# Optimization experiments

Hardware: AMD Instinct MI355X
Metric: run time of the kernel (lower is better)

The kernel has to match this reference:

```python
import jax, jax.numpy as jnp
import numpy as np

# hyperparameters from init_kwargs
TEMP = 0.05
MOMENTUM = 0.2
ALPHA = 0.9
TEMP_DIST = 0.6
LAMBDA1 = 1.0
LAMBDA2 = 1.0
EPS_CONS = 2.0
NUM_SAMPLES = 8192
NUM_FEATURES = 2048
B = 256
K = 20
EPS = 1e-12


def setup_inputs() -> dict:
    key = jax.random.key(0)
    ks = jax.random.split(key, 8)
    inputs0 = jax.random.normal(ks[0], (B, NUM_FEATURES), dtype=jnp.float32)
    logits0 = jax.random.normal(ks[1], (B, NUM_SAMPLES), dtype=jnp.float32)
    logits1 = jax.random.normal(ks[2], (B, NUM_SAMPLES), dtype=jnp.float32)
    targets = jax.random.randint(ks[3], (B,), 0, NUM_SAMPLES, dtype=jnp.int32)
    indexes = jnp.arange(B, dtype=jnp.int32)  # global idx == batch idx (identity idx2bidx)
    neighbors = jax.random.randint(ks[4], (B, K), 0, B, dtype=jnp.int32)
    neighbor_dists = jax.random.uniform(ks[5], (B, K), dtype=jnp.float32)
    rampup = jnp.ones((), dtype=jnp.float32)
    features = jax.random.normal(ks[6], (NUM_SAMPLES, NUM_FEATURES), dtype=jnp.float32)
    features = features / jnp.linalg.norm(features, axis=1, keepdims=True)
    return {
        'inputs0': inputs0, 'logits0': logits0, 'logits1': logits1,
        'targets': targets, 'indexes': indexes, 'neighbors': neighbors,
        'neighbor_dists': neighbor_dists, 'rampup': rampup, 'features': features,
    }


def reference(inputs0, logits0, logits1, targets, indexes, neighbors,
              neighbor_dists, rampup, features):
    # F.normalize(inputs[0], dim=1)
    x = inputs0 / jnp.maximum(jnp.linalg.norm(inputs0, axis=1, keepdims=True), EPS)

    # CM forward: scores against memory bank, scaled by temperature
    outputs = (x @ features.T) / TEMP                      # [B, S]
    logp = jax.nn.log_softmax(outputs, axis=-1)
    loss_nce = -jnp.mean(jnp.take_along_axis(logp, targets[:, None], axis=1))

    targets_onehot = jax.nn.one_hot(targets, NUM_SAMPLES, dtype=logits0.dtype)

    # neighbor gathering: indexes = arange(B) so idx2bidx is identity; every
    # neighbor in [0,B) passes the `nb in indexes` filter.
    p0 = jax.nn.softmax(logits0, axis=-1)[neighbors]       # [B, K, S]
    p1 = jax.nn.softmax(logits1, axis=-1)[neighbors]       # [B, K, S]
    # loop appends logits0-row then logits1-row per neighbor -> interleave
    p = jnp.stack([p0, p1], axis=2).reshape(B, 2 * K, NUM_SAMPLES)
    d2 = jnp.repeat(neighbor_dists, 2, axis=1)             # [B, 2K] (d,d pairs)
    w = jax.nn.softmax(d2 / TEMP_DIST, axis=1)             # [B, 2K]
    logits_neighbors1 = jnp.einsum('bk,bks->bs', w, p)     # [B, S]

    # KL branch: neighbors with dist <= eps_consistency (all, since eps=2.0)
    mask = (neighbor_dists <= EPS_CONS).astype(p0.dtype)   # [B, K]
    cnt = jnp.maximum(mask.sum(axis=1, keepdims=True), 1.0)
    logits_neighbors1_KL = jnp.einsum('bk,bks->bs', mask, p0) / cnt  # [B, S]

    refined = ALPHA * targets_onehot + (1.0 - ALPHA) * jax.lax.stop_gradient(logits_neighbors1)
    loss_ce = jnp.mean(jnp.sum(-refined * jax.nn.log_softmax(logits0, axis=-1), axis=1))

    # KLDivLoss(logsoftmax(logits1).detach(), target) with batchmean reduction
    lp1 = jax.lax.stop_gradient(jax.nn.log_softmax(logits1, axis=-1))
    t = logits_neighbors1_KL
    kl = jnp.sum(jnp.where(t > 0, t * (jnp.log(jnp.maximum(t, EPS)) - lp1), 0.0)) / B

    # CM momentum memory-bank scatter update (backward side-effect in torch);
    # equivalent to the sequential loop when targets are unique in the batch.
    upd = MOMENTUM * features[targets] + (1.0 - MOMENTUM) * x
    upd = upd / jnp.maximum(jnp.linalg.norm(upd, axis=1, keepdims=True), EPS)
    new_features = features.at[targets].set(upd)

    return (loss_nce, LAMBDA1 * loss_ce, LAMBDA2 * rampup * kl, new_features)
```

## Files before the change

### kernel.cpp

```cpp
#include <hip/hip_runtime.h>
#include <cmath>

#define NB 256
#define NS 8192
#define NF 2048
#define NK 20

typedef _Float16 half8 __attribute__((ext_vector_type(8)));
typedef _Float16 half4 __attribute__((ext_vector_type(4)));
typedef float f32x4 __attribute__((ext_vector_type(4)));

__device__ __forceinline__ void async16(const void* g, void* l) {
  __builtin_amdgcn_global_load_lds(
      (const __attribute__((address_space(1))) unsigned int*)g,
      (__attribute__((address_space(3))) unsigned int*)l, 16, 0, 0);
}

__device__ __forceinline__ float waveSum(float v) {
#pragma unroll
  for (int off = 32; off > 0; off >>= 1) v += __shfl_xor(v, off, 64);
  return v;
}
__device__ __forceinline__ float waveMax(float v) {
#pragma unroll
  for (int off = 32; off > 0; off >>= 1) v = fmaxf(v, __shfl_xor(v, off, 64));
  return v;
}

__global__ __launch_bounds__(256, 1) void prep(
    const float4* __restrict__ f4, const float* __restrict__ in0,
    const float* __restrict__ logits0, const float* __restrict__ logits1,
    const int* __restrict__ targets, const int* __restrict__ neighbors,
    const float* __restrict__ ndist,
    float* __restrict__ outF, _Float16* __restrict__ fh,
    _Float16* __restrict__ Pt, _Float16* __restrict__ xh,
    _Float16* __restrict__ alpha_h, float* __restrict__ mll,
    _Float16* __restrict__ Wp) {
  __shared__ alignas(16) union {
    struct {
      float redA[4];
      float redB[4];
      unsigned long long wmask[4];
    } s;
    _Float16 Lt[32 * 520];
  } sm;
  int tid = threadIdx.x, blk = blockIdx.x;
  int wave = tid >> 6, lane = tid & 63;

  if (blk < NS) {
    int row = blk;
    const float4* fr = f4 + (size_t)row * (NF / 4);
    float4 v0 = fr[tid], v1 = fr[tid + 256];
    half4 h0, h1;
    h0[0] = (_Float16)v0.x; h0[1] = (_Float16)v0.y; h0[2] = (_Float16)v0.z; h0[3] = (_Float16)v0.w;
    h1[0] = (_Float16)v1.x; h1[1] = (_Float16)v1.y; h1[2] = (_Float16)v1.z; h1[3] = (_Float16)v1.w;
    ((half4*)(fh + (size_t)row * NF))[tid] = h0;
    ((half4*)(fh + (size_t)row * NF))[tid + 256] = h1;
    unsigned long long mk = __ballot(targets[tid] == row);
    if (lane == 0) sm.s.wmask[wave] = mk;
    __syncthreads();
    int u = -1;
#pragma unroll
    for (int w = 3; w >= 0; --w)
      if (u < 0 && sm.s.wmask[w])
        u = w * 64 + 63 - (int)__clzll(sm.s.wmask[w]);
    if (u >= 0) {
      const float4* xr = (const float4*)(in0 + (size_t)u * NF);
      float4 a0 = xr[tid], a1 = xr[tid + 256];
      float ssx = a0.x * a0.x + a0.y * a0.y + a0.z * a0.z + a0.w * a0.w +
                  a1.x * a1.x + a1.y * a1.y + a1.z * a1.z + a1.w * a1.w;
      float w1 = waveSum(ssx);
      if (lane == 0) sm.s.redA[wave] = w1;
      __syncthreads();
      float totx = (sm.s.redA[0] + sm.s.redA[1]) + (sm.s.redA[2] + sm.s.redA[3]);
      float ix = 0.8f / fmaxf(sqrtf(totx), 1e-12f);
      v0 = make_float4(0.2f * v0.x + ix * a0.x, 0.2f * v0.y + ix * a0.y,
                       0.2f * v0.z + ix * a0.z, 0.2f * v0.w + ix * a0.w);
      v1 = make_float4(0.2f * v1.x + ix * a1.x, 0.2f * v1.y + ix * a1.y,
                       0.2f * v1.z + ix * a1.z, 0.2f * v1.w + ix * a1.w);
      float ss = v0.x * v0.x + v0.y * v0.y + v0.z * v0.z + v0.w * v0.w +
                 v1.x * v1.x + v1.y * v1.y + v1.z * v1.z + v1.w * v1.w;
      float w2 = waveSum(ss);
      if (lane == 0) sm.s.redB[wave] = w2;
      __syncthreads();
      float tot = (sm.s.redB[0] + sm.s.redB[1]) + (sm.s.redB[2] + sm.s.redB[3]);
      float inv = 1.0f / fmaxf(sqrtf(tot), 1e-12f);
      v0.x *= inv; v0.y *= inv; v0.z *= inv; v0.w *= inv;
      v1.x *= inv; v1.y *= inv; v1.z *= inv; v1.w *= inv;
    }
    float* o = outF + (size_t)row * NF;
    int e0 = tid * 4, e1 = 1024 + tid * 4;
    o[e0 + 0] = v0.x; o[e0 + 1] = v0.y; o[e0 + 2] = v0.z; o[e0 + 3] = v0.w;
    o[e1 + 0] = v1.x; o[e1 + 1] = v1.y; o[e1 + 2] = v1.z; o[e1 + 3] = v1.w;
  } else if (blk < NS + 512) {
    int r = blk - NS;
    const float* src = (r < NB) ? logits0 : logits1;
    const float4* row = (const float4*)(src + (size_t)(r & (NB - 1)) * NS);
    float4 v[8];
    float mx = -1e30f;
#pragma unroll
    for (int i = 0; i < 8; ++i) {
      v[i] = row[tid + i * 256];
      mx = fmaxf(mx, fmaxf(fmaxf(v[i].x, v[i].y), fmaxf(v[i].z, v[i].w)));
    }
    float wv = waveMax(mx);
    if (lane == 0) sm.s.redA[wave] = wv;
    __syncthreads();
    float m = fmaxf(fmaxf(sm.s.redA[0], sm.s.redA[1]), fmaxf(sm.s.redA[2], sm.s.redA[3]));
    float se = 0.0f;
#pragma unroll
    for (int i = 0; i < 8; ++i)
      se += expf(v[i].x - m) + expf(v[i].y - m) + expf(v[i].z - m) + expf(v[i].w - m);
    float sw = waveSum(se);
    if (lane == 0) sm.s.redB[wave] = sw;
    __syncthreads();
    float l = (sm.s.redB[0] + sm.s.redB[1]) + (sm.s.redB[2] + sm.s.redB[3]);
    if (tid == 0) {
      mll[r] = m + logf(l);
      alpha_h[r] = (_Float16)(256.0f * expf(-m) / l);
    }
  } else if (blk < NS + 768) {
    int s0 = (blk - (NS + 512)) * 32;
#pragma unroll
    for (int g = 0; g < 16; ++g) {
      int pos = g * 256 + tid;
      int row = pos >> 3, c4 = pos & 7;
      const float* src = ((row < NB) ? logits0 + (size_t)row * NS
                                     : logits1 + (size_t)(row - NB) * NS) + s0 + c4 * 4;
      float4 v = *(const float4*)src;
      sm.Lt[(c4 * 4 + 0) * 520 + row] = (_Float16)expf(v.x);
      sm.Lt[(c4 * 4 + 1) * 520 + row] = (_Float16)expf(v.y);
      sm.Lt[(c4 * 4 + 2) * 520 + row] = (_Float16)expf(v.z);
      sm.Lt[(c4 * 4 + 3) * 520 + row] = (_Float16)expf(v.w);
    }
    __syncthreads();
    int srow = tid >> 3, seg = tid & 7;
    _Float16* dst = Pt + (size_t)(s0 + srow) * 512 + seg * 64;
    const _Float16* lsrc = &sm.Lt[srow * 520 + seg * 64];
#pragma unroll
    for (int q = 0; q < 8; ++q)
      *(half8*)(dst + q * 8) = *(const half8*)(lsrc + q * 8);
  } else if (blk < NS + 1024) {
    int b = blk - (NS + 768);
    const float4* row = (const float4*)(in0 + (size_t)b * NF);
    float4 v0 = row[tid], v1 = row[tid + 256];
    float ss = v0.x * v0.x + v0.y * v0.y + v0.z * v0.z + v0.w * v0.w +
               v1.x * v1.x + v1.y * v1.y + v1.z * v1.z + v1.w * v1.w;
    float w = waveSum(ss);
    if (lane == 0) sm.s.redA[wave] = w;
    __syncthreads();
    float tot = (sm.s.redA[0] + sm.s.redA[1]) + (sm.s.redA[2] + sm.s.redA[3]);
    float inv = 1.0f / fmaxf(sqrtf(tot), 1e-12f);
    half4 h0, h1;
    h0[0] = (_Float16)(v0.x * inv); h0[1] = (_Float16)(v0.y * inv);
    h0[2] = (_Float16)(v0.z * inv); h0[3] = (_Float16)(v0.w * inv);
    h1[0] = (_Float16)(v1.x * inv); h1[1] = (_Float16)(v1.y * inv);
    h1[2] = (_Float16)(v1.z * inv); h1[3] = (_Float16)(v1.w * inv);
    ((half4*)(xh + (size_t)b * NF))[tid] = h0;
    ((half4*)(xh + (size_t)b * NF))[tid + 256] = h1;
  } else {
    float4* W4 = (float4*)Wp;
    for (int i = tid; i < 512 * 512 * 2 / 16; i += 256) W4[i] = make_float4(0, 0, 0, 0);
    __syncthreads();
    int b = tid;
    float d[NK], e[NK];
    int n[NK];
    float s = 0.0f;
    int cnt = 0;
#pragma unroll
    for (int k = 0; k < NK; ++k) {
      d[k] = ndist[b * NK + k];
      n[k] = neighbors[b * NK + k];
      e[k] = expf(d[k] * (1.0f / 0.6f));
      s += e[k];
      cnt += (d[k] <= 2.0f) ? 1 : 0;
    }
    float invs = 1.0f / (2.0f * s);
    float invc = 1.0f / fmaxf((float)cnt, 1.0f);
    _Float16* rkl = Wp + (size_t)b * 512;
    _Float16* rce = Wp + (size_t)(256 + b) * 512;
#pragma unroll
    for (int k = 0; k < NK; ++k) {
      bool first = true;
#pragma unroll
      for (int k2 = 0; k2 < NK; ++k2)
        if (k2 < k && n[k2] == n[k]) first = false;
      if (first) {
        float wsum = 0.0f, ksum = 0.0f;
#pragma unroll
        for (int k2 = 0; k2 < NK; ++k2)
          if (k2 >= k && n[k2] == n[k]) {
            wsum += e[k2] * invs;
            ksum += (d[k2] <= 2.0f) ? invc : 0.0f;
          }
        rkl[n[k]] = (_Float16)ksum;
        rce[n[k]] = (_Float16)wsum;
        rce[256 + n[k]] = (_Float16)wsum;
      }
    }
  }
}

__global__ __launch_bounds__(256) void gemms(
    const _Float16* __restrict__ xh, const _Float16* __restrict__ fh,
    const _Float16* __restrict__ Wp, const _Float16* __restrict__ Pt,
    const _Float16* __restrict__ alpha_h,
    const float* __restrict__ logits0, const float* __restrict__ logits1,
    const float* __restrict__ mll, const int* __restrict__ targets,
    float* __restrict__ pm, float* __restrict__ pl, float* __restrict__ tgt,
    float* __restrict__ part) {
  __shared__ alignas(16) _Float16 As[128 * 64];
  __shared__ alignas(16) _Float16 Bs[128 * 64];
  __shared__ alignas(16) _Float16 Al[512];
  __shared__ float red[4];
  int tid = threadIdx.x, wave = tid >> 6, lane = tid & 63;
  int quad = lane >> 4, r16 = lane & 15, lrow = lane >> 3, lch = lane & 7;
  int blk = blockIdx.x;
  if (blk < 256) {
    int bx = blk & 127, by = blk >> 7;
    int n0 = bx * 64, m0 = by * 128;
    f32x4 acc[2][4] = {};
    for (int k0 = 0; k0 < NF; k0 += 64) {
      __syncthreads();
#pragma unroll
      for (int ss = 0; ss < 4; ++ss) {
        int rl = ss * 32 + wave * 8 + lrow;
        int sc = lch ^ (rl & 7);
        async16(xh + (size_t)(m0 + rl) * NF + k0 + sc * 8, &As[rl * 64 + lch * 8]);
      }
#pragma unroll
      for (int ss = 0; ss < 2; ++ss) {
        int rl = ss * 32 + wave * 8 + lrow;
        int sc = lch ^ (rl & 7);
        async16(fh + (size_t)(n0 + rl) * NF + k0 + sc * 8, &Bs[rl * 64 + lch * 8]);
      }
      __syncthreads();
#pragma unroll
      for (int sub = 0; sub < 2; ++sub) {
        int slot = ((sub * 4 + quad) ^ (r16 & 7)) * 8;
        half8 af[2], bf[4];
#pragma unroll
        for (int i = 0; i < 2; ++i)
          af[i] = *(const half8*)&As[(wave * 32 + i * 16 + r16) * 64 + slot];
#pragma unroll
        for (int j = 0; j < 4; ++j)
          bf[j] = *(const half8*)&Bs[(j * 16 + r16) * 64 + slot];
#pragma unroll
        for (int i = 0; i < 2; ++i)
#pragma unroll
          for (int j = 0; j < 4; ++j)
            acc[i][j] = __builtin_amdgcn_mfma_f32_16x16x32_f16(af[i], bf[j], acc[i][j], 0, 0, 0);
      }
    }
#pragma unroll
    for (int i = 0; i < 2; ++i)
#pragma unroll
      for (int r = 0; r < 4; ++r) {
        int R = m0 + wave * 32 + i * 16 + quad * 4 + r;
        float sv[4];
#pragma unroll
        for (int j = 0; j < 4; ++j) sv[j] = acc[i][j][r] * 20.0f;
        float mx = fmaxf(fmaxf(sv[0], sv[1]), fmaxf(sv[2], sv[3]));
#pragma unroll
        for (int m2 = 1; m2 < 16; m2 <<= 1) mx = fmaxf(mx, __shfl_xor(mx, m2, 64));
        float e = expf(sv[0] - mx) + expf(sv[1] - mx) + expf(sv[2] - mx) + expf(sv[3] - mx);
#pragma unroll
        for (int m2 = 1; m2 < 16; m2 <<= 1) e += __shfl_xor(e, m2, 64);
        int tg = targets[R];
#pragma unroll
        for (int j = 0; j < 4; ++j)
          if (n0 + j * 16 + r16 == tg) tgt[R] = sv[j];
        if (r16 == 0) { pm[R * 128 + bx] = mx; pl[R * 128 + bx] = e; }
      }
  } else {
    int nb = blk - 256;
    int bx = nb & 63, by = nb >> 6;
    int n0 = bx * 128, m0 = by * 128;
    int wm = (wave >> 1) * 64, wn = (wave & 1) * 64;
    if (tid < 64) ((half8*)Al)[tid] = ((const half8*)alpha_h)[tid];
    f32x4 acc[4][4] = {};
    for (int k0 = 0; k0 < 512; k0 += 64) {
      __syncthreads();
#pragma unroll
      for (int ss = 0; ss < 4; ++ss) {
        int rl = ss * 32 + wave * 8 + lrow;
        int sc = lch ^ (rl & 7);
        async16(Wp + (size_t)(m0 + rl) * 512 + k0 + sc * 8, &As[rl * 64 + lch * 8]);
        async16(Pt + (size_t)(n0 + rl) * 512 + k0 + sc * 8, &Bs[rl * 64 + lch * 8]);
      }
      __syncthreads();
#pragma unroll
      for (int sub = 0; sub < 2; ++sub) {
        int slot = ((sub * 4 + quad) ^ (r16 & 7)) * 8;
        half8 alv = *(const half8*)&Al[k0 + slot];
        half8 af[4], bf[4];
#pragma unroll
        for (int i = 0; i < 4; ++i)
          af[i] = *(const half8*)&As[(wm + i * 16 + r16) * 64 + slot];
#pragma unroll
        for (int j = 0; j < 4; ++j)
          bf[j] = *(const half8*)&Bs[(wn + j * 16 + r16) * 64 + slot] * alv;
#pragma unroll
        for (int i = 0; i < 4; ++i)
#pragma unroll
          for (int j = 0; j < 4; ++j)
            acc[i][j] = __builtin_amdgcn_mfma_f32_16x16x32_f16(af[i], bf[j], acc[i][j], 0, 0, 0);
      }
    }
    bool iskl = (by < 2);
    const float* lgbase = iskl ? logits1 : logits0;
    float local = 0.0f;
#pragma unroll
    for (int i = 0; i < 4; ++i)
#pragma unroll
      for (int r = 0; r < 4; ++r) {
        int Mg = m0 + wm + i * 16 + quad * 4 + r;
        int b = iskl ? Mg : (Mg - 256);
        float mv = mll[iskl ? 256 + b : b];
        const float* lgrow = lgbase + (size_t)b * NS + n0 + wn;
#pragma unroll
        for (int j = 0; j < 4; ++j) {
          float lg = lgrow[j * 16 + r16];
          float t = acc[i][j][r] * (1.0f / 256.0f);
          if (iskl)
            local += (t > 0.0f) ? t * (logf(fmaxf(t, 1e-12f)) - (lg - mv)) : 0.0f;
          else
            local += -0.1f * t * (lg - mv);
        }
      }
    float wsv = waveSum(local);
    if (lane == 0) red[wave] = wsv;
    __syncthreads();
    if (tid == 0) part[nb] = (red[0] + red[1]) + (red[2] + red[3]);
  }
}

__global__ __launch_bounds__(256) void final_reduce(
    const float* __restrict__ pm, const float* __restrict__ pl,
    const float* __restrict__ tgt, const float* __restrict__ part,
    const float* __restrict__ logits0, const float* __restrict__ mll,
    const int* __restrict__ targets, const float* __restrict__ rampup,
    float* __restrict__ out) {
  __shared__ float rA[4], rB[4], rC[4], rD[4];
  int tid = threadIdx.x, wave = tid >> 6, lane = tid & 63;
  int b = tid;
  const float* pmb = pm + b * 128;
  const float* plb = pl + b * 128;
  float mx = -1e30f;
  for (int s = 0; s < 128; ++s) mx = fmaxf(mx, pmb[s]);
  float S = 0.0f;
  for (int s = 0; s < 128; ++s) S += plb[s] * expf(pmb[s] - mx);
  float nce = -(tgt[b] - mx - logf(S));
  int tg = targets[b];
  float oh = -0.9f * (logits0[(size_t)b * NS + tg] - mll[b]);
  float c = part[tid];
  float klc = (tid < 128) ? c : 0.0f;
  float cec = (tid < 128) ? 0.0f : c;
  float wn_ = waveSum(nce), wo = waveSum(oh), wk = waveSum(klc), wc = waveSum(cec);
  if (lane == 0) { rA[wave] = wn_; rB[wave] = wo; rC[wave] = wk; rD[wave] = wc; }
  __syncthreads();
  if (tid == 0) {
    float sn = rA[0] + rA[1] + rA[2] + rA[3];
    float so = rB[0] + rB[1] + rB[2] + rB[3];
    float sk = rC[0] + rC[1] + rC[2] + rC[3];
    float sc2 = rD[0] + rD[1] + rD[2] + rD[3];
    out[0] = sn * (1.0f / 256.0f);
    out[1] = (so + sc2) * (1.0f / 256.0f);
    out[2] = rampup[0] * sk * (1.0f / 256.0f);
  }
}

extern "C" void kernel_launch(void* const* d_in, const int* in_sizes, int n_in,
                              void* d_out, int out_size, void* d_ws, size_t ws_size,
                              hipStream_t stream) {
  const float* inputs0 = (const float*)d_in[0];
  const float* logits0 = (const float*)d_in[1];
  const float* logits1 = (const float*)d_in[2];
  const int* targets = (const int*)d_in[3];
  const int* neighbors = (const int*)d_in[5];
  const float* ndist = (const float*)d_in[6];
  const float* rampup = (const float*)d_in[7];
  const float* features = (const float*)d_in[8];
  float* out = (float*)d_out;

  char* ws = (char*)d_ws;
  float* mll = (float*)(ws + 4096);
  _Float16* alpha_h = (_Float16*)(ws + 8192);
  float* part = (float*)(ws + 12288);
  float* tgt = (float*)(ws + 16384);
  float* pm = (float*)(ws + 65536);
  float* pl = (float*)(ws + 196608);
  _Float16* Wp = (_Float16*)(ws + 524288);
  _Float16* xh = (_Float16*)(ws + (3 << 20));
  _Float16* Pt = (_Float16*)(ws + (4 << 20));
  _Float16* fh = (_Float16*)(ws + (12 << 20));

  prep<<<NS + 1025, 256, 0, stream>>>((const float4*)features, inputs0, logits0,
                                      logits1, targets, neighbors, ndist,
                                      out + 3, fh, Pt, xh, alpha_h, mll, Wp);
  gemms<<<512, 256, 0, stream>>>(xh, fh, Wp, Pt, alpha_h, logits0, logits1, mll,
                                 targets, pm, pl, tgt, part);
  final_reduce<<<1, 256, 0, stream>>>(pm, pl, tgt, part, logits0, mll, targets,
                                      rampup, out);
}
```

Before: 220.3 us.

## Parallelize final reduction across blocks with atomics and split transpose blocks finer

The final loss reduction moves from a single 256-thread block, where each thread serially looped over 128 partials, to 256 blocks of 128 threads. Each block reduces one batch row with wave shuffles and accumulates into the outputs with atomicAdd; the outputs are zeroed inside prep. The logits exp/transpose stage now uses 512 blocks of 16 columns instead of 256 blocks of 32, which halves the shared tile and gives more parallel blocks. The memory-bank writeback is vectorized to float4 stores. Atomics make the summation order nondeterministic.

```diff
diff --git a/kernel.cpp b/kernel.cpp
--- a/kernel.cpp
+++ b/kernel.cpp
@@ -35,14 +35,14 @@
     float* __restrict__ outF, _Float16* __restrict__ fh,
     _Float16* __restrict__ Pt, _Float16* __restrict__ xh,
     _Float16* __restrict__ alpha_h, float* __restrict__ mll,
-    _Float16* __restrict__ Wp) {
+    _Float16* __restrict__ Wp, float* __restrict__ loss) {
   __shared__ alignas(16) union {
     struct {
       float redA[4];
       float redB[4];
       unsigned long long wmask[4];
     } s;
-    _Float16 Lt[32 * 520];
+    _Float16 Lt[16 * 520];
   } sm;
   int tid = threadIdx.x, blk = blockIdx.x;
   int wave = tid >> 6, lane = tid & 63;
@@ -88,10 +88,9 @@
       v0.x *= inv; v0.y *= inv; v0.z *= inv; v0.w *= inv;
       v1.x *= inv; v1.y *= inv; v1.z *= inv; v1.w *= inv;
     }
-    float* o = outF + (size_t)row * NF;
-    int e0 = tid * 4, e1 = 1024 + tid * 4;
-    o[e0 + 0] = v0.x; o[e0 + 1] = v0.y; o[e0 + 2] = v0.z; o[e0 + 3] = v0.w;
-    o[e1 + 0] = v1.x; o[e1 + 1] = v1.y; o[e1 + 2] = v1.z; o[e1 + 3] = v1.w;
+    float4* o4 = (float4*)(outF + (size_t)row * NF);
+    o4[tid] = v0;
+    o4[tid + 256] = v1;
   } else if (blk < NS + 512) {
     int r = blk - NS;
     const float* src = (r < NB) ? logits0 : logits1;
@@ -119,12 +118,12 @@
       mll[r] = m + logf(l);
       alpha_h[r] = (_Float16)(256.0f * expf(-m) / l);
     }
-  } else if (blk < NS + 768) {
-    int s0 = (blk - (NS + 512)) * 32;
-#pragma unroll
-    for (int g = 0; g < 16; ++g) {
+  } else if (blk < NS + 1024) {
+    int s0 = (blk - (NS + 512)) * 16;
+#pragma unroll
+    for (int g = 0; g < 8; ++g) {
       int pos = g * 256 + tid;
-      int row = pos >> 3, c4 = pos & 7;
+      int row = pos >> 2, c4 = pos & 3;
       const float* src = ((row < NB) ? logits0 + (size_t)row * NS
                                      : logits1 + (size_t)(row - NB) * NS) + s0 + c4 * 4;
       float4 v = *(const float4*)src;
@@ -134,14 +133,14 @@
       sm.Lt[(c4 * 4 + 3) * 520 + row] = (_Float16)expf(v.w);
     }
     __syncthreads();
-    int srow = tid >> 3, seg = tid & 7;
-    _Float16* dst = Pt + (size_t)(s0 + srow) * 512 + seg * 64;
-    const _Float16* lsrc = &sm.Lt[srow * 520 + seg * 64];
-#pragma unroll
-    for (int q = 0; q < 8; ++q)
+    int srow = tid >> 4, seg = tid & 15;
+    _Float16* dst = Pt + (size_t)(s0 + srow) * 512 + seg * 32;
+    const _Float16* lsrc = &sm.Lt[srow * 520 + seg * 32];
+#pragma unroll
+    for (int q = 0; q < 4; ++q)
       *(half8*)(dst + q * 8) = *(const half8*)(lsrc + q * 8);
-  } else if (blk < NS + 1024) {
-    int b = blk - (NS + 768);
+  } else if (blk < NS + 1280) {
+    int b = blk - (NS + 1024);
     const float4* row = (const float4*)(in0 + (size_t)b * NF);
     float4 v0 = row[tid], v1 = row[tid + 256];
     float ss = v0.x * v0.x + v0.y * v0.y + v0.z * v0.z + v0.w * v0.w +
@@ -159,6 +158,7 @@
     ((half4*)(xh + (size_t)b * NF))[tid] = h0;
     ((half4*)(xh + (size_t)b * NF))[tid + 256] = h1;
   } else {
+    if (tid < 3) loss[tid] = 0.0f;
     float4* W4 = (float4*)Wp;
     for (int i = tid; i < 512 * 512 * 2 / 16; i += 256) W4[i] = make_float4(0, 0, 0, 0);
     __syncthreads();
@@ -335,38 +335,36 @@
   }
 }
 
-__global__ __launch_bounds__(256) void final_reduce(
+__global__ __launch_bounds__(128) void final_reduce(
     const float* __restrict__ pm, const float* __restrict__ pl,
     const float* __restrict__ tgt, const float* __restrict__ part,
     const float* __restrict__ logits0, const float* __restrict__ mll,
     const int* __restrict__ targets, const float* __restrict__ rampup,
     float* __restrict__ out) {
-  __shared__ float rA[4], rB[4], rC[4], rD[4];
-  int tid = threadIdx.x, wave = tid >> 6, lane = tid & 63;
-  int b = tid;
-  const float* pmb = pm + b * 128;
-  const float* plb = pl + b * 128;
-  float mx = -1e30f;
-  for (int s = 0; s < 128; ++s) mx = fmaxf(mx, pmb[s]);
-  float S = 0.0f;
-  for (int s = 0; s < 128; ++s) S += plb[s] * expf(pmb[s] - mx);
-  float nce = -(tgt[b] - mx - logf(S));
-  int tg = targets[b];
-  float oh = -0.9f * (logits0[(size_t)b * NS + tg] - mll[b]);
-  float c = part[tid];
-  float klc = (tid < 128) ? c : 0.0f;
-  float cec = (tid < 128) ? 0.0f : c;
-  float wn_ = waveSum(nce), wo = waveSum(oh), wk = waveSum(klc), wc = waveSum(cec);
-  if (lane == 0) { rA[wave] = wn_; rB[wave] = wo; rC[wave] = wk; rD[wave] = wc; }
+  __shared__ float rmx[2], rsm[2];
+  int tid = threadIdx.x;
+  int b = blockIdx.x;
+  float m = pm[b * 128 + tid];
+  float l = pl[b * 128 + tid];
+  float wm = waveMax(m);
+  if ((tid & 63) == 0) rmx[tid >> 6] = wm;
+  __syncthreads();
+  float mx = fmaxf(rmx[0], rmx[1]);
+  float e = l * expf(m - mx);
+  float ws = waveSum(e);
+  if ((tid & 63) == 0) rsm[tid >> 6] = ws;
   __syncthreads();
   if (tid == 0) {
-    float sn = rA[0] + rA[1] + rA[2] + rA[3];
-    float so = rB[0] + rB[1] + rB[2] + rB[3];
-    float sk = rC[0] + rC[1] + rC[2] + rC[3];
-    float sc2 = rD[0] + rD[1] + rD[2] + rD[3];
-    out[0] = sn * (1.0f / 256.0f);
-    out[1] = (so + sc2) * (1.0f / 256.0f);
-    out[2] = rampup[0] * sk * (1.0f / 256.0f);
+    float S = rsm[0] + rsm[1];
+    float nce = -(tgt[b] - mx - logf(S));
+    int tg = targets[b];
+    float oh = -0.9f * (logits0[(size_t)b * NS + tg] - mll[b]);
+    float pb = part[b];
+    float v1 = oh;
+    if (b >= 128) v1 += pb;
+    atomicAdd(out + 0, nce * (1.0f / 256.0f));
+    atomicAdd(out + 1, v1 * (1.0f / 256.0f));
+    if (b < 128) atomicAdd(out + 2, rampup[0] * pb * (1.0f / 256.0f));
   }
 }
 
@@ -395,11 +393,11 @@
   _Float16* Pt = (_Float16*)(ws + (4 << 20));
   _Float16* fh = (_Float16*)(ws + (12 << 20));
 
-  prep<<<NS + 1025, 256, 0, stream>>>((const float4*)features, inputs0, logits0,
+  prep<<<NS + 1281, 256, 0, stream>>>((const float4*)features, inputs0, logits0,
                                       logits1, targets, neighbors, ndist,
-                                      out + 3, fh, Pt, xh, alpha_h, mll, Wp);
+                                      out + 3, fh, Pt, xh, alpha_h, mll, Wp, out);
   gemms<<<512, 256, 0, stream>>>(xh, fh, Wp, Pt, alpha_h, logits0, logits1, mll,
                                  targets, pm, pl, tgt, part);
-  final_reduce<<<1, 256, 0, stream>>>(pm, pl, tgt, part, logits0, mll, targets,
-                                      rampup, out);
-}
+  final_reduce<<<256, 128, 0, stream>>>(pm, pl, tgt, part, logits0, mll, targets,
+                                        rampup, out);
+}
```

New measurement: 211.4 us. -4.0%, faster.
